# Kernel optimization log

Measured on AMD Instinct MI355X. Metric: run time of the kernel, lower is better.

The kernel has to match this reference:

```python
import jax, jax.numpy as jnp
import numpy as np

B, R, D = 16, 2048, 512
H2, NREL = 2 * D, 2048  # relation_mlp hidden = 2*d_model, output = n_relations
MIN_PROB = 0.1          # early-stop probability threshold from the torch code


def setup_inputs() -> dict:
    key = jax.random.key(0)
    ks = jax.random.split(key, 8)
    sc = lambda k, shp: jax.random.normal(k, shp, jnp.float32) * 0.02
    return {
        "rel_encoding": jax.random.normal(ks[0], (B, R, D), jnp.float32),
        "na_emb": jax.random.normal(ks[1], (D,), jnp.float32),
        "v_w": sc(ks[2], (D, D)), "v_b": jnp.zeros((D,), jnp.float32),
        "o_w": sc(ks[3], (D, D)), "o_b": jnp.zeros((D,), jnp.float32),
        "ln_g": jnp.ones((D,), jnp.float32), "ln_b": jnp.zeros((D,), jnp.float32),
        "w1": sc(ks[4], (H2, D)), "b1": jnp.zeros((H2,), jnp.float32),
        "w2": sc(ks[5], (NREL, H2)), "b2": jnp.zeros((NREL,), jnp.float32),
    }


def _ln(x, g, b, eps=1e-5):
    m = jnp.mean(x, axis=-1, keepdims=True)
    v = jnp.var(x, axis=-1, keepdims=True)
    return (x - m) * jax.lax.rsqrt(v + eps) * g + b


def reference(rel_encoding, na_emb, v_w, v_b, o_w, o_b, ln_g, ln_b, w1, b1, w2, b2):
    # Cross-attention with a single key/value token: softmax over a length-1 axis
    # is identically 1, so attn_out = out_proj(v_proj(kv)) for every query position.
    x = rel_encoding                                         # [B,R,D]
    attn = (x @ v_w.T + v_b) @ o_w.T + o_b                   # [B,R,D]

    def step_logits(state):                                  # state broadcasts to [B,R,D]
        h = _ln(attn + state, ln_g, ln_b)                    # residual + layernorm
        return jax.nn.relu(h @ w1.T + b1) @ w2.T + b2        # [B,R,NREL]

    # step 0: query is the na_embedding
    p0 = jax.nn.softmax(step_logits(na_emb), axis=-1)
    m0 = jnp.max(p0, axis=-1)
    i0 = jnp.argmax(p0, axis=-1)
    cont0 = (i0 != 0) & (m0 >= MIN_PROB)                     # else break before step 0 emits

    # step 1: last appended state is the relation encoding itself
    p1 = jax.nn.softmax(step_logits(x), axis=-1)
    m1 = jnp.max(p1, axis=-1)
    i1 = jnp.argmax(p1, axis=-1)
    cont1 = cont0 & (i1 != 0) & (m1 >= MIN_PROB)

    # rule_score = prod of accepted step probs; 0.0 if no step accepted
    scores = jnp.where(cont0, jnp.where(cont1, m0 * m1, m0), 0.0)  # [B,R]
    lengths = cont0.astype(jnp.int32) + cont1.astype(jnp.int32)    # ragged rule lengths
    return scores, i0, i1, lengths
```

## Files before the change

kernel.cpp:

```cpp
#include <hip/hip_runtime.h>
#include <math.h>

#define MTOT 32768
#define DD   512
#define HHD  1024
#define NRELN 2048
#define SCA  64.f
#define SCB  1024.f
#define INVS (1.f / 65536.f)

typedef _Float16 h8  __attribute__((ext_vector_type(8)));
typedef float    f16v __attribute__((ext_vector_type(16)));

__device__ __forceinline__ void fsplit(float x, _Float16& h, _Float16& l) {
  _Float16 t = (_Float16)x;
  h = t;
  l = (_Float16)(x - (float)t);
}

__device__ __forceinline__ void omerge(float& M, float& S, int& I, float m2, float s2, int i2) {
  if (m2 > M || (m2 == M && i2 < I)) { S = S * __expf(M - m2) + s2; M = m2; I = i2; }
  else                               { S += s2 * __expf(m2 - M); }
}

__device__ __forceinline__ void gld16(const _Float16* g, _Float16* l) {
  __builtin_amdgcn_global_load_lds(
      (const __attribute__((address_space(1))) void*)g,
      (__attribute__((address_space(3))) void*)l, 16, 0, 0);
}


__global__ void prep_wvo_split(const float* __restrict__ vw, const float* __restrict__ ow,
                               _Float16* __restrict__ wh, _Float16* __restrict__ wl) {
  int idx = blockIdx.x * 256 + threadIdx.x;
  int k = idx & 511;
  int n = idx >> 9;
  float s = 0.f;
  for (int j = 0; j < DD; ++j) s += ow[n * DD + j] * vw[j * DD + k];
  fsplit(s * SCB, wh[n * DD + k], wl[n * DD + k]);
}

__global__ void prep_cvec(const float* __restrict__ ow, const float* __restrict__ vb,
                          const float* __restrict__ ob, float* __restrict__ c) {
  int i = blockIdx.x * 256 + threadIdx.x;
  if (i < DD) {
    float s = ob[i];
    for (int k = 0; k < DD; ++k) s += ow[i * DD + k] * vb[k];
    c[i] = s;
  }
}

__global__ void prep_w1p_split(const float* __restrict__ w1, const float* __restrict__ g,
                               _Float16* __restrict__ wh, _Float16* __restrict__ wl) {
  int idx = blockIdx.x * 256 + threadIdx.x;
  int k = idx & 511;
  int n = idx >> 9;
  fsplit(w1[n * DD + k] * g[k] * SCB, wh[n * DD + k], wl[n * DD + k]);
}

__global__ void prep_b1p(const float* __restrict__ w1, const float* __restrict__ lnb,
                         const float* __restrict__ b1, float* __restrict__ b1p) {
  int n = blockIdx.x * 256 + threadIdx.x;
  if (n < HHD) {
    float s = b1[n];
    for (int k = 0; k < DD; ++k) s += w1[n * DD + k] * lnb[k];
    b1p[n] = s;
  }
}

__global__ void prep_w2_split(const float* __restrict__ w2,
                              _Float16* __restrict__ wh, _Float16* __restrict__ wl) {
  int idx = blockIdx.x * 256 + threadIdx.x;
  int k = idx & 1023;
  int n = idx >> 10;
  fsplit(w2[n * HHD + k] * SCB, wh[n * HHD + k], wl[n * HHD + k]);
}

__global__ void split_x(const float* __restrict__ src, _Float16* __restrict__ h,
                        _Float16* __restrict__ l) {
  int idx = (blockIdx.x * 256 + threadIdx.x) * 8;
  float4 a = *(const float4*)(src + idx);
  float4 b = *(const float4*)(src + idx + 4);
  float vv[8] = {a.x, a.y, a.z, a.w, b.x, b.y, b.z, b.w};
  _Float16 hh[8], ll[8];
#pragma unroll
  for (int i = 0; i < 8; ++i) fsplit(vv[i] * SCA, hh[i], ll[i]);
  *(h8*)(h + idx) = *(h8*)hh;
  *(h8*)(l + idx) = *(h8*)ll;
}

template <int MODE, int KDIM, int NTOT>
__global__ __launch_bounds__(256) void gemm_split(
    const _Float16* __restrict__ Ah, const _Float16* __restrict__ Al,
    const _Float16* __restrict__ Bh, const _Float16* __restrict__ Bl,
    const float* __restrict__ bias,
    float* __restrict__ outF,
    _Float16* __restrict__ outHh, _Float16* __restrict__ outHl,
    float* __restrict__ pM, float* __restrict__ pS, float* __restrict__ pI,
    int row0) {
  __shared__ __align__(16) _Float16 sA[2][128][32];
  __shared__ __align__(16) _Float16 sB[2][128][32];
  const int t = threadIdx.x;
  const int lane = t & 63;
  const int wv = t >> 6;
  const int wr = wv & 1, wc = wv >> 1;
  const int l31 = lane & 31, half = lane >> 5;
  const int m0 = blockIdx.x << 7;
  const int n0 = blockIdx.y << 7;

  const _Float16* gsp = (wv == 0) ? Ah : (wv == 1) ? Al : (wv == 2) ? Bh : Bl;
  const int gb = (wv < 2) ? m0 : n0;
  _Float16* lbase = (wv == 0) ? &sA[0][0][0] : (wv == 1) ? &sA[1][0][0]
                  : (wv == 2) ? &sB[0][0][0] : &sB[1][0][0];
  const int srow = lane >> 2;
  const int schunk = (lane & 3) ^ ((lane >> 3) & 3);
  const _Float16* gptr0 = gsp + (size_t)(gb + srow) * KDIM + schunk * 8;

  f16v acc[2][2] = {};
  const int swz = (lane >> 1) & 3;

  for (int k0 = 0; k0 < KDIM; k0 += 32) {
    __syncthreads();
#pragma unroll
    for (int it = 0; it < 8; ++it)
      gld16(gptr0 + k0 + (size_t)(it * 16) * KDIM, lbase + it * 512);
    __syncthreads();
#pragma unroll
    for (int ks = 0; ks < 2; ++ks) {
      const int pos = (((ks << 1) + half) ^ swz) << 3;
      h8 af_h[2], af_l[2], bf_h[2], bf_l[2];
#pragma unroll
      for (int i = 0; i < 2; ++i) {
        const int mr = wr * 64 + i * 32 + l31;
        af_h[i] = *(const h8*)&sA[0][mr][pos];
        af_l[i] = *(const h8*)&sA[1][mr][pos];
      }
#pragma unroll
      for (int j = 0; j < 2; ++j) {
        const int nr = wc * 64 + j * 32 + l31;
        bf_h[j] = *(const h8*)&sB[0][nr][pos];
        bf_l[j] = *(const h8*)&sB[1][nr][pos];
      }
#pragma unroll
      for (int j = 0; j < 2; ++j)
#pragma unroll
        for (int i = 0; i < 2; ++i) {
          acc[i][j] = __builtin_amdgcn_mfma_f32_32x32x16_f16(af_h[i], bf_h[j], acc[i][j], 0, 0, 0);
          acc[i][j] = __builtin_amdgcn_mfma_f32_32x32x16_f16(af_h[i], bf_l[j], acc[i][j], 0, 0, 0);
          acc[i][j] = __builtin_amdgcn_mfma_f32_32x32x16_f16(af_l[i], bf_h[j], acc[i][j], 0, 0, 0);
        }
    }
  }

  float bb[2];
  int gc[2];
#pragma unroll
  for (int j = 0; j < 2; ++j) {
    gc[j] = n0 + wc * 64 + j * 32 + l31;
    bb[j] = bias[gc[j]];
  }
  if constexpr (MODE == 0) {
#pragma unroll
    for (int i = 0; i < 2; ++i)
#pragma unroll
      for (int r = 0; r < 16; ++r) {
        const int row = m0 + wr * 64 + i * 32 + (r & 3) + 8 * (r >> 2) + 4 * half;
#pragma unroll
        for (int j = 0; j < 2; ++j)
          outF[(size_t)row * NTOT + gc[j]] = acc[i][j][r] * INVS + bb[j];
      }
  } else if constexpr (MODE == 1) {
#pragma unroll
    for (int i = 0; i < 2; ++i)
#pragma unroll
      for (int r = 0; r < 16; ++r) {
        const int row = m0 + wr * 64 + i * 32 + (r & 3) + 8 * (r >> 2) + 4 * half;
#pragma unroll
        for (int j = 0; j < 2; ++j) {
          float v = fmaxf(acc[i][j][r] * INVS + bb[j], 0.f) * SCA;
          _Float16 hh, ll;
          fsplit(v, hh, ll);
          outHh[(size_t)row * NTOT + gc[j]] = hh;
          outHl[(size_t)row * NTOT + gc[j]] = ll;
        }
      }
  } else {
    const int slot = blockIdx.y * 2 + wc;
#pragma unroll
    for (int i = 0; i < 2; ++i)
#pragma unroll
      for (int r = 0; r < 16; ++r) {
        float v0 = acc[i][0][r] * INVS + bb[0];
        float v1 = acc[i][1][r] * INVS + bb[1];
        float M;
        int I;
        if (v0 >= v1) { M = v0; I = gc[0]; }
        else          { M = v1; I = gc[1]; }
#pragma unroll
        for (int sh = 1; sh <= 16; sh <<= 1) {
          float M2 = __shfl_xor(M, sh);
          int   I2 = __shfl_xor(I, sh);
          if (M2 > M || (M2 == M && I2 < I)) { M = M2; I = I2; }
        }
        float S = __expf(v0 - M) + __expf(v1 - M);
#pragma unroll
        for (int sh = 1; sh <= 16; sh <<= 1) S += __shfl_xor(S, sh);
        if (l31 == 0) {
          const int grow = row0 + m0 + wr * 64 + i * 32 + (r & 3) + 8 * (r >> 2) + 4 * half;
          pM[(size_t)slot * MTOT + grow] = M;
          pS[(size_t)slot * MTOT + grow] = S;
          pI[(size_t)slot * MTOT + grow] = (float)I;
        }
      }
  }
}

__global__ __launch_bounds__(256) void ln_dual(
    const float* __restrict__ A, const float* __restrict__ X,
    const float* __restrict__ na,
    _Float16* __restrict__ y0h, _Float16* __restrict__ y0l,
    _Float16* __restrict__ y1h, _Float16* __restrict__ y1l, int row0) {
  int t = threadIdx.x;
  int lane = t & 63;
  int w = t >> 6;
  int r = blockIdx.x * 4 + w;
  const float* ap = A + (size_t)r * DD + lane * 8;
  const float* xp = X + (size_t)(row0 + r) * DD + lane * 8;
  const float* np = na + lane * 8;
  float v0[8], v1[8];
  float s0 = 0.f, q0 = 0.f, s1 = 0.f, q1 = 0.f;
#pragma unroll
  for (int i = 0; i < 8; ++i) {
    float a = ap[i];
    v0[i] = a + np[i];
    v1[i] = a + xp[i];
    s0 += v0[i]; q0 += v0[i] * v0[i];
    s1 += v1[i]; q1 += v1[i] * v1[i];
  }
#pragma unroll
  for (int m = 1; m <= 32; m <<= 1) {
    s0 += __shfl_xor(s0, m); q0 += __shfl_xor(q0, m);
    s1 += __shfl_xor(s1, m); q1 += __shfl_xor(q1, m);
  }
  float mu0 = s0 * (1.f / DD), mu1 = s1 * (1.f / DD);
  float rs0 = 1.f / sqrtf(q0 * (1.f / DD) - mu0 * mu0 + 1e-5f);
  float rs1 = 1.f / sqrtf(q1 * (1.f / DD) - mu1 * mu1 + 1e-5f);
  _Float16 h0[8], l0[8], h1[8], l1[8];
#pragma unroll
  for (int i = 0; i < 8; ++i) {
    fsplit((v0[i] - mu0) * rs0 * SCA, h0[i], l0[i]);
    fsplit((v1[i] - mu1) * rs1 * SCA, h1[i], l1[i]);
  }
  *(h8*)(y0h + (size_t)r * DD + lane * 8) = *(h8*)h0;
  *(h8*)(y0l + (size_t)r * DD + lane * 8) = *(h8*)l0;
  *(h8*)(y1h + (size_t)r * DD + lane * 8) = *(h8*)h1;
  *(h8*)(y1l + (size_t)r * DD + lane * 8) = *(h8*)l1;
}

__global__ void finalize_k(const float* __restrict__ pM0, const float* __restrict__ pS0,
                           const float* __restrict__ pI0, const float* __restrict__ pM1,
                           const float* __restrict__ pS1, const float* __restrict__ pI1,
                           float* __restrict__ out) {
  int r = blockIdx.x * 256 + threadIdx.x;
  float M = pM0[r], S = pS0[r];
  int I = (int)pI0[r];
  for (int s = 1; s < 32; ++s) {
    size_t o = (size_t)s * MTOT + r;
    omerge(M, S, I, pM0[o], pS0[o], (int)pI0[o]);
  }
  float m0v = 1.f / S;
  int i0v = I;
  M = pM1[r]; S = pS1[r]; I = (int)pI1[r];
  for (int s = 1; s < 32; ++s) {
    size_t o = (size_t)s * MTOT + r;
    omerge(M, S, I, pM1[o], pS1[o], (int)pI1[o]);
  }
  float m1v = 1.f / S;
  int i1v = I;
  bool c0 = (i0v != 0) && (m0v >= 0.1f);
  bool c1 = c0 && (i1v != 0) && (m1v >= 0.1f);
  out[r] = c0 ? (c1 ? m0v * m1v : m0v) : 0.f;
  out[MTOT + r] = (float)i0v;
  out[2 * MTOT + r] = (float)i1v;
  out[3 * MTOT + r] = (float)((c0 ? 1 : 0) + (c1 ? 1 : 0));
}

extern "C" void kernel_launch(void* const* d_in, const int* in_sizes, int n_in,
                              void* d_out, int out_size, void* d_ws, size_t ws_size,
                              hipStream_t stream) {
  const float* X   = (const float*)d_in[0];
  const float* na  = (const float*)d_in[1];
  const float* vw  = (const float*)d_in[2];
  const float* vb  = (const float*)d_in[3];
  const float* ow  = (const float*)d_in[4];
  const float* ob  = (const float*)d_in[5];
  const float* lng = (const float*)d_in[6];
  const float* lnb = (const float*)d_in[7];
  const float* w1  = (const float*)d_in[8];
  const float* b1  = (const float*)d_in[9];
  const float* w2  = (const float*)d_in[10];
  const float* b2  = (const float*)d_in[11];
  float* out = (float*)d_out;

  char* p = (char*)d_ws;
  auto alloc = [&](size_t bytes) -> void* {
    void* r = (void*)p;
    p += (bytes + 255) & ~(size_t)255;
    return r;
  };
  _Float16* wvo_h = (_Float16*)alloc(512 * 512 * 2);
  _Float16* wvo_l = (_Float16*)alloc(512 * 512 * 2);
  float*    cvec  = (float*)alloc(512 * 4);
  _Float16* w1p_h = (_Float16*)alloc(1024 * 512 * 2);
  _Float16* w1p_l = (_Float16*)alloc(1024 * 512 * 2);
  float*    b1p   = (float*)alloc(1024 * 4);
  _Float16* w2_h  = (_Float16*)alloc(2048 * 1024 * 2);
  _Float16* w2_l  = (_Float16*)alloc(2048 * 1024 * 2);
  float* pM0 = (float*)alloc((size_t)32 * MTOT * 4);
  float* pS0 = (float*)alloc((size_t)32 * MTOT * 4);
  float* pI0 = (float*)alloc((size_t)32 * MTOT * 4);
  float* pM1 = (float*)alloc((size_t)32 * MTOT * 4);
  float* pS1 = (float*)alloc((size_t)32 * MTOT * 4);
  float* pI1 = (float*)alloc((size_t)32 * MTOT * 4);
  size_t fixed = (size_t)(p - (char*)d_ws);
  size_t remain = ws_size > fixed + 8192 ? ws_size - fixed - 8192 : 0;
  int chunk = (int)(remain / 10240);
  chunk &= ~127;
  if (chunk < 128) chunk = 128;
  if (chunk > MTOT) chunk = MTOT;
  _Float16* xs_h = (_Float16*)alloc((size_t)chunk * 512 * 2);
  _Float16* xs_l = (_Float16*)alloc((size_t)chunk * 512 * 2);
  float*    Abuf = (float*)alloc((size_t)chunk * 512 * 4);
  _Float16* y0_h = (_Float16*)alloc((size_t)chunk * 512 * 2);
  _Float16* y0_l = (_Float16*)alloc((size_t)chunk * 512 * 2);
  _Float16* H_h  = (_Float16*)alloc((size_t)chunk * 1024 * 2);
  _Float16* H_l  = (_Float16*)alloc((size_t)chunk * 1024 * 2);
  _Float16* y1_h = xs_h;
  _Float16* y1_l = xs_l;

  prep_wvo_split<<<1024, 256, 0, stream>>>(vw, ow, wvo_h, wvo_l);
  prep_cvec<<<2, 256, 0, stream>>>(ow, vb, ob, cvec);
  prep_w1p_split<<<2048, 256, 0, stream>>>(w1, lng, w1p_h, w1p_l);
  prep_b1p<<<4, 256, 0, stream>>>(w1, lnb, b1, b1p);
  prep_w2_split<<<8192, 256, 0, stream>>>(w2, w2_h, w2_l);

  for (int row0 = 0; row0 < MTOT; row0 += chunk) {
    int rows = (MTOT - row0 < chunk) ? (MTOT - row0) : chunk;
    split_x<<<rows / 4, 256, 0, stream>>>(X + (size_t)row0 * 512, xs_h, xs_l);
    gemm_split<0, 512, 512><<<dim3(rows / 128, 4), 256, 0, stream>>>(
        xs_h, xs_l, wvo_h, wvo_l, cvec, Abuf, nullptr, nullptr,
        nullptr, nullptr, nullptr, 0);
    ln_dual<<<rows / 4, 256, 0, stream>>>(Abuf, X, na, y0_h, y0_l, y1_h, y1_l, row0);
    for (int s = 0; s < 2; ++s) {
      gemm_split<1, 512, 1024><<<dim3(rows / 128, 8), 256, 0, stream>>>(
          s == 0 ? y0_h : y1_h, s == 0 ? y0_l : y1_l, w1p_h, w1p_l, b1p,
          nullptr, H_h, H_l, nullptr, nullptr, nullptr, 0);
      gemm_split<2, 1024, 2048><<<dim3(rows / 128, 16), 256, 0, stream>>>(
          H_h, H_l, w2_h, w2_l, b2, nullptr, nullptr, nullptr,
          s == 0 ? pM0 : pM1, s == 0 ? pS0 : pS1, s == 0 ? pI0 : pI1, row0);
    }
  }
  finalize_k<<<MTOT / 256, 256, 0, stream>>>(pM0, pS0, pI0, pM1, pS1, pI1, out);
}
```

Measured before the change: 1.680 ms.

## Compute final GEMM in single fp16, recompute near-tie rows in split precision

The largest GEMM (hidden to relation logits) now runs as one fp16 MFMA pass instead of three split-precision passes. It tracks the top-two logits and the softmax sum per row. Rows whose top-two margin is below a threshold are flagged with an atomic counter, gathered into a compact buffer, and recomputed with the full split-precision GEMM to settle the argmax. Max-probability values still come from the approximate pass, and rescue is capped at a fixed number of rows per chunk, so accuracy depends on logit gaps and the cap. The LDS swizzle also changes, and the final reduction moves into per-chunk flag kernels.

New measurement: 1.635 ms. -2.7%, faster.

```diff
diff --git a/kernel.cpp b/kernel.cpp
--- a/kernel.cpp
+++ b/kernel.cpp
@@ -8,6 +8,8 @@
 #define SCA  64.f
 #define SCB  1024.f
 #define INVS (1.f / 65536.f)
+#define CAPR 4096
+#define MARGIN 2.0e-3f
 
 typedef _Float16 h8  __attribute__((ext_vector_type(8)));
 typedef float    f16v __attribute__((ext_vector_type(16)));
@@ -16,11 +18,6 @@
   _Float16 t = (_Float16)x;
   h = t;
   l = (_Float16)(x - (float)t);
-}
-
-__device__ __forceinline__ void omerge(float& M, float& S, int& I, float m2, float s2, int i2) {
-  if (m2 > M || (m2 == M && i2 < I)) { S = S * __expf(M - m2) + s2; M = m2; I = i2; }
-  else                               { S += s2 * __expf(m2 - M); }
 }
 
 __device__ __forceinline__ void gld16(const _Float16* g, _Float16* l) {
@@ -89,6 +86,8 @@
   *(h8*)(l + idx) = *(h8*)ll;
 }
 
+__global__ void zero_cnt(int* c) { c[blockIdx.x * 256 + threadIdx.x] = 0; }
+
 template <int MODE, int KDIM, int NTOT>
 __global__ __launch_bounds__(256) void gemm_split(
     const _Float16* __restrict__ Ah, const _Float16* __restrict__ Al,
@@ -96,8 +95,8 @@
     const float* __restrict__ bias,
     float* __restrict__ outF,
     _Float16* __restrict__ outHh, _Float16* __restrict__ outHl,
-    float* __restrict__ pM, float* __restrict__ pS, float* __restrict__ pI,
-    int row0) {
+    float* __restrict__ pM, float* __restrict__ pI,
+    const int* __restrict__ cntp, int pstr) {
   __shared__ __align__(16) _Float16 sA[2][128][32];
   __shared__ __align__(16) _Float16 sB[2][128][32];
   const int t = threadIdx.x;
@@ -105,127 +104,299 @@
   const int wv = t >> 6;
   const int wr = wv & 1, wc = wv >> 1;
   const int l31 = lane & 31, half = lane >> 5;
-  const int m0 = blockIdx.x << 7;
   const int n0 = blockIdx.y << 7;
 
   const _Float16* gsp = (wv == 0) ? Ah : (wv == 1) ? Al : (wv == 2) ? Bh : Bl;
-  const int gb = (wv < 2) ? m0 : n0;
   _Float16* lbase = (wv == 0) ? &sA[0][0][0] : (wv == 1) ? &sA[1][0][0]
                   : (wv == 2) ? &sB[0][0][0] : &sB[1][0][0];
   const int srow = lane >> 2;
-  const int schunk = (lane & 3) ^ ((lane >> 3) & 3);
-  const _Float16* gptr0 = gsp + (size_t)(gb + srow) * KDIM + schunk * 8;
-
-  f16v acc[2][2] = {};
-  const int swz = (lane >> 1) & 3;
-
-  for (int k0 = 0; k0 < KDIM; k0 += 32) {
+  const int scp = lane & 3;
+  const int swzE = ((srow >> 1) & 3) ^ ((srow >> 3) & 1);
+  const int swzO = swzE ^ 2;
+  const int swz = ((l31 >> 1) ^ (l31 >> 3)) & 3;
+
+  int nmb;
+  if constexpr (MODE == 2) {
+    int a = *cntp;
+    if (a > CAPR) a = CAPR;
+    nmb = (a + 127) >> 7;
+  } else {
+    nmb = gridDim.x;
+  }
+
+  for (int mb = blockIdx.x; mb < nmb; mb += gridDim.x) {
+    const int m0 = mb << 7;
+    const int gb = (wv < 2) ? m0 : n0;
+    const _Float16* gA0 = gsp + (size_t)(gb + srow) * KDIM + ((scp ^ swzE) << 3);
+    const _Float16* gA1 = gsp + (size_t)(gb + srow) * KDIM + ((scp ^ swzO) << 3);
+
+    f16v acc[2][2] = {};
+    for (int k0 = 0; k0 < KDIM; k0 += 32) {
+      __syncthreads();
+#pragma unroll
+      for (int it = 0; it < 8; ++it)
+        gld16(((it & 1) ? gA1 : gA0) + (size_t)(it * 16) * KDIM + k0, lbase + it * 512);
+      __syncthreads();
+#pragma unroll
+      for (int ks = 0; ks < 2; ++ks) {
+        const int pos = (((ks << 1) + half) ^ swz) << 3;
+        h8 af_h[2], af_l[2], bf_h[2], bf_l[2];
+#pragma unroll
+        for (int i = 0; i < 2; ++i) {
+          const int mr = wr * 64 + i * 32 + l31;
+          af_h[i] = *(const h8*)&sA[0][mr][pos];
+          af_l[i] = *(const h8*)&sA[1][mr][pos];
+        }
+#pragma unroll
+        for (int j = 0; j < 2; ++j) {
+          const int nr = wc * 64 + j * 32 + l31;
+          bf_h[j] = *(const h8*)&sB[0][nr][pos];
+          bf_l[j] = *(const h8*)&sB[1][nr][pos];
+        }
+#pragma unroll
+        for (int j = 0; j < 2; ++j)
+#pragma unroll
+          for (int i = 0; i < 2; ++i) {
+            acc[i][j] = __builtin_amdgcn_mfma_f32_32x32x16_f16(af_h[i], bf_h[j], acc[i][j], 0, 0, 0);
+            acc[i][j] = __builtin_amdgcn_mfma_f32_32x32x16_f16(af_h[i], bf_l[j], acc[i][j], 0, 0, 0);
+            acc[i][j] = __builtin_amdgcn_mfma_f32_32x32x16_f16(af_l[i], bf_h[j], acc[i][j], 0, 0, 0);
+          }
+      }
+    }
+
+    float bb[2];
+    int gc[2];
+#pragma unroll
+    for (int j = 0; j < 2; ++j) {
+      gc[j] = n0 + wc * 64 + j * 32 + l31;
+      bb[j] = bias[gc[j]];
+    }
+    if constexpr (MODE == 0) {
+#pragma unroll
+      for (int i = 0; i < 2; ++i)
+#pragma unroll
+        for (int r = 0; r < 16; ++r) {
+          const int row = m0 + wr * 64 + i * 32 + (r & 3) + 8 * (r >> 2) + 4 * half;
+#pragma unroll
+          for (int j = 0; j < 2; ++j)
+            outF[(size_t)row * NTOT + gc[j]] = acc[i][j][r] * INVS + bb[j];
+        }
+    } else if constexpr (MODE == 1) {
+#pragma unroll
+      for (int i = 0; i < 2; ++i)
+#pragma unroll
+        for (int r = 0; r < 16; ++r) {
+          const int row = m0 + wr * 64 + i * 32 + (r & 3) + 8 * (r >> 2) + 4 * half;
+#pragma unroll
+          for (int j = 0; j < 2; ++j) {
+            float v = fmaxf(acc[i][j][r] * INVS + bb[j], 0.f) * SCA;
+            _Float16 hh, ll;
+            fsplit(v, hh, ll);
+            outHh[(size_t)row * NTOT + gc[j]] = hh;
+            outHl[(size_t)row * NTOT + gc[j]] = ll;
+          }
+        }
+    } else {
+      const int slot = blockIdx.y * 2 + wc;
+#pragma unroll
+      for (int i = 0; i < 2; ++i)
+#pragma unroll
+        for (int r = 0; r < 16; ++r) {
+          float v0 = acc[i][0][r] * INVS + bb[0];
+          float v1 = acc[i][1][r] * INVS + bb[1];
+          float M;
+          int I;
+          if (v0 >= v1) { M = v0; I = gc[0]; }
+          else          { M = v1; I = gc[1]; }
+#pragma unroll
+          for (int sh = 1; sh <= 16; sh <<= 1) {
+            float M2 = __shfl_xor(M, sh);
+            int   I2 = __shfl_xor(I, sh);
+            if (M2 > M || (M2 == M && I2 < I)) { M = M2; I = I2; }
+          }
+          if (l31 == 0) {
+            const int grow = m0 + wr * 64 + i * 32 + (r & 3) + 8 * (r >> 2) + 4 * half;
+            pM[(size_t)slot * pstr + grow] = M;
+            pI[(size_t)slot * pstr + grow] = (float)I;
+          }
+        }
+    }
+  }
+}
+
+__global__ __launch_bounds__(256) void gemm_approx(
+    const _Float16* __restrict__ Ah, const _Float16* __restrict__ Bh,
+    const float* __restrict__ bias,
+    float* __restrict__ pM, float* __restrict__ pM2,
+    float* __restrict__ pS, int* __restrict__ pI, int astr) {
+  __shared__ __align__(16) _Float16 sAB[12288];
+  const int t = threadIdx.x;
+  const int lane = t & 63;
+  const int wv = t >> 6;
+  const int wr = wv & 1, wc = wv >> 1;
+  const int l31 = lane & 31, half = lane >> 5;
+  const int m0 = blockIdx.x << 7;
+  const int n0 = blockIdx.y << 8;
+
+  const _Float16* gsrc[6];
+  _Float16* ldst[6];
+#pragma unroll
+  for (int it = 0; it < 6; ++it) {
+    int p = (it * 4 + wv) * 64 + lane;
+    const _Float16* s;
+    if (p < 512) {
+      int row = p >> 2, cp = p & 3;
+      int sw = ((row >> 1) ^ (row >> 3)) & 3;
+      s = Ah + (size_t)(m0 + row) * HHD + ((cp ^ sw) << 3);
+    } else {
+      int pq = p - 512;
+      int row = pq >> 2, cp = pq & 3;
+      int sw = ((row >> 1) ^ (row >> 3)) & 3;
+      s = Bh + (size_t)(n0 + row) * HHD + ((cp ^ sw) << 3);
+    }
+    gsrc[it] = s;
+    ldst[it] = sAB + (size_t)(it * 4 + wv) * 512;
+  }
+  const int swz = ((l31 >> 1) ^ (l31 >> 3)) & 3;
+
+  f16v acc[2][4] = {};
+  for (int k0 = 0; k0 < HHD; k0 += 32) {
     __syncthreads();
 #pragma unroll
-    for (int it = 0; it < 8; ++it)
-      gld16(gptr0 + k0 + (size_t)(it * 16) * KDIM, lbase + it * 512);
+    for (int it = 0; it < 6; ++it) gld16(gsrc[it] + k0, ldst[it]);
     __syncthreads();
 #pragma unroll
     for (int ks = 0; ks < 2; ++ks) {
       const int pos = (((ks << 1) + half) ^ swz) << 3;
-      h8 af_h[2], af_l[2], bf_h[2], bf_l[2];
-#pragma unroll
-      for (int i = 0; i < 2; ++i) {
-        const int mr = wr * 64 + i * 32 + l31;
-        af_h[i] = *(const h8*)&sA[0][mr][pos];
-        af_l[i] = *(const h8*)&sA[1][mr][pos];
+      h8 af[2], bf[4];
+#pragma unroll
+      for (int i = 0; i < 2; ++i)
+        af[i] = *(const h8*)&sAB[(size_t)(wr * 64 + i * 32 + l31) * 32 + pos];
+#pragma unroll
+      for (int j = 0; j < 4; ++j)
+        bf[j] = *(const h8*)&sAB[4096 + (size_t)(wc * 128 + j * 32 + l31) * 32 + pos];
+#pragma unroll
+      for (int j = 0; j < 4; ++j)
+#pragma unroll
+        for (int i = 0; i < 2; ++i)
+          acc[i][j] = __builtin_amdgcn_mfma_f32_32x32x16_f16(af[i], bf[j], acc[i][j], 0, 0, 0);
+    }
+  }
+
+  const int slot = blockIdx.y * 2 + wc;
+  float bb[4];
+  int gc[4];
+#pragma unroll
+  for (int j = 0; j < 4; ++j) {
+    gc[j] = n0 + wc * 128 + j * 32 + l31;
+    bb[j] = bias[gc[j]];
+  }
+#pragma unroll
+  for (int i = 0; i < 2; ++i)
+#pragma unroll
+    for (int r = 0; r < 16; ++r) {
+      float M = acc[i][0][r] * INVS + bb[0], M2 = -INFINITY, S = 1.f;
+      int I = gc[0];
+#pragma unroll
+      for (int j = 1; j < 4; ++j) {
+        float v = acc[i][j][r] * INVS + bb[j];
+        if (v > M || (v == M && gc[j] < I)) {
+          S = S * __expf(M - v) + 1.f; M2 = M; M = v; I = gc[j];
+        } else {
+          S += __expf(v - M); M2 = fmaxf(M2, v);
+        }
       }
 #pragma unroll
-      for (int j = 0; j < 2; ++j) {
-        const int nr = wc * 64 + j * 32 + l31;
-        bf_h[j] = *(const h8*)&sB[0][nr][pos];
-        bf_l[j] = *(const h8*)&sB[1][nr][pos];
+      for (int sh = 1; sh <= 16; sh <<= 1) {
+        float Mo = __shfl_xor(M, sh);
+        float M2o = __shfl_xor(M2, sh);
+        float So = __shfl_xor(S, sh);
+        int   Io = __shfl_xor(I, sh);
+        if (Mo > M || (Mo == M && Io < I)) {
+          S = S * __expf(M - Mo) + So; M2 = fmaxf(M, M2o); M = Mo; I = Io;
+        } else {
+          S += So * __expf(Mo - M); M2 = fmaxf(M2, Mo);
+        }
       }
-#pragma unroll
-      for (int j = 0; j < 2; ++j)
-#pragma unroll
-        for (int i = 0; i < 2; ++i) {
-          acc[i][j] = __builtin_amdgcn_mfma_f32_32x32x16_f16(af_h[i], bf_h[j], acc[i][j], 0, 0, 0);
-          acc[i][j] = __builtin_amdgcn_mfma_f32_32x32x16_f16(af_h[i], bf_l[j], acc[i][j], 0, 0, 0);
-          acc[i][j] = __builtin_amdgcn_mfma_f32_32x32x16_f16(af_l[i], bf_h[j], acc[i][j], 0, 0, 0);
-        }
-    }
-  }
-
-  float bb[2];
-  int gc[2];
-#pragma unroll
-  for (int j = 0; j < 2; ++j) {
-    gc[j] = n0 + wc * 64 + j * 32 + l31;
-    bb[j] = bias[gc[j]];
-  }
-  if constexpr (MODE == 0) {
-#pragma unroll
-    for (int i = 0; i < 2; ++i)
-#pragma unroll
-      for (int r = 0; r < 16; ++r) {
-        const int row = m0 + wr * 64 + i * 32 + (r & 3) + 8 * (r >> 2) + 4 * half;
-#pragma unroll
-        for (int j = 0; j < 2; ++j)
-          outF[(size_t)row * NTOT + gc[j]] = acc[i][j][r] * INVS + bb[j];
+      if (l31 == 0) {
+        const int grow = m0 + wr * 64 + i * 32 + (r & 3) + 8 * (r >> 2) + 4 * half;
+        pM[(size_t)slot * astr + grow] = M;
+        pM2[(size_t)slot * astr + grow] = M2;
+        pS[(size_t)slot * astr + grow] = S;
+        pI[(size_t)slot * astr + grow] = I;
       }
-  } else if constexpr (MODE == 1) {
-#pragma unroll
-    for (int i = 0; i < 2; ++i)
-#pragma unroll
-      for (int r = 0; r < 16; ++r) {
-        const int row = m0 + wr * 64 + i * 32 + (r & 3) + 8 * (r >> 2) + 4 * half;
-#pragma unroll
-        for (int j = 0; j < 2; ++j) {
-          float v = fmaxf(acc[i][j][r] * INVS + bb[j], 0.f) * SCA;
-          _Float16 hh, ll;
-          fsplit(v, hh, ll);
-          outHh[(size_t)row * NTOT + gc[j]] = hh;
-          outHl[(size_t)row * NTOT + gc[j]] = ll;
-        }
-      }
-  } else {
-    const int slot = blockIdx.y * 2 + wc;
-#pragma unroll
-    for (int i = 0; i < 2; ++i)
-#pragma unroll
-      for (int r = 0; r < 16; ++r) {
-        float v0 = acc[i][0][r] * INVS + bb[0];
-        float v1 = acc[i][1][r] * INVS + bb[1];
-        float M;
-        int I;
-        if (v0 >= v1) { M = v0; I = gc[0]; }
-        else          { M = v1; I = gc[1]; }
-#pragma unroll
-        for (int sh = 1; sh <= 16; sh <<= 1) {
-          float M2 = __shfl_xor(M, sh);
-          int   I2 = __shfl_xor(I, sh);
-          if (M2 > M || (M2 == M && I2 < I)) { M = M2; I = I2; }
-        }
-        float S = __expf(v0 - M) + __expf(v1 - M);
-#pragma unroll
-        for (int sh = 1; sh <= 16; sh <<= 1) S += __shfl_xor(S, sh);
-        if (l31 == 0) {
-          const int grow = row0 + m0 + wr * 64 + i * 32 + (r & 3) + 8 * (r >> 2) + 4 * half;
-          pM[(size_t)slot * MTOT + grow] = M;
-          pS[(size_t)slot * MTOT + grow] = S;
-          pI[(size_t)slot * MTOT + grow] = (float)I;
-        }
-      }
-  }
+    }
+}
+
+__global__ void flag_k(const float* __restrict__ pM, const float* __restrict__ pM2,
+                       const float* __restrict__ pS, const int* __restrict__ pI,
+                       int astr, int rows,
+                       float* __restrict__ map, int* __restrict__ iap, int row0,
+                       int* __restrict__ list, int* __restrict__ cnt) {
+  int r = blockIdx.x * 256 + threadIdx.x;
+  if (r >= rows) return;
+  float M = pM[r], M2 = pM2[r], S = pS[r];
+  int I = pI[r];
+  for (int s = 1; s < 16; ++s) {
+    size_t o = (size_t)s * astr + r;
+    float m = pM[o], m2 = pM2[o], ss = pS[o];
+    int ii = pI[o];
+    if (m > M || (m == M && ii < I)) {
+      M2 = fmaxf(M, m2); S = S * __expf(M - m) + ss; M = m; I = ii;
+    } else {
+      M2 = fmaxf(M2, m); S += ss * __expf(m - M);
+    }
+  }
+  map[row0 + r] = 1.f / S;
+  iap[row0 + r] = I;
+  if (M - M2 < MARGIN) {
+    int c = atomicAdd(cnt, 1);
+    if (c < CAPR) list[c] = r;
+  }
+}
+
+__global__ void gather_k(const _Float16* __restrict__ Hh, const _Float16* __restrict__ Hl,
+                         const int* __restrict__ list, const int* __restrict__ cnt,
+                         _Float16* __restrict__ Gh, _Float16* __restrict__ Gl) {
+  int b = blockIdx.x;
+  int active = *cnt;
+  if (active > CAPR) active = CAPR;
+  if (b >= active) return;
+  int r = list[b];
+  int t = threadIdx.x;
+  *(h8*)(Gh + (size_t)b * HHD + t * 8) = *(const h8*)(Hh + (size_t)r * HHD + t * 8);
+  *(h8*)(Gl + (size_t)b * HHD + t * 8) = *(const h8*)(Hl + (size_t)r * HHD + t * 8);
+}
+
+__global__ void rescue_merge(const float* __restrict__ pMr, const float* __restrict__ pIr,
+                             const int* __restrict__ list, const int* __restrict__ cnt,
+                             int* __restrict__ iap, int row0) {
+  int c = blockIdx.x * 256 + threadIdx.x;
+  int a = *cnt;
+  if (a > CAPR) a = CAPR;
+  if (c >= a) return;
+  float M = pMr[c];
+  int I = (int)pIr[c];
+  for (int s = 1; s < 32; ++s) {
+    size_t o = (size_t)s * CAPR + c;
+    float m = pMr[o];
+    int i2 = (int)pIr[o];
+    if (m > M || (m == M && i2 < I)) { M = m; I = i2; }
+  }
+  iap[row0 + list[c]] = I;
 }
 
 __global__ __launch_bounds__(256) void ln_dual(
     const float* __restrict__ A, const float* __restrict__ X,
     const float* __restrict__ na,
     _Float16* __restrict__ y0h, _Float16* __restrict__ y0l,
-    _Float16* __restrict__ y1h, _Float16* __restrict__ y1l, int row0) {
+    _Float16* __restrict__ y1h, _Float16* __restrict__ y1l) {
   int t = threadIdx.x;
   int lane = t & 63;
   int w = t >> 6;
   int r = blockIdx.x * 4 + w;
   const float* ap = A + (size_t)r * DD + lane * 8;
-  const float* xp = X + (size_t)(row0 + r) * DD + lane * 8;
+  const float* xp = X + (size_t)r * DD + lane * 8;
   const float* np = na + lane * 8;
   float v0[8], v1[8];
   float s0 = 0.f, q0 = 0.f, s1 = 0.f, q1 = 0.f;
@@ -257,26 +428,12 @@
   *(h8*)(y1l + (size_t)r * DD + lane * 8) = *(h8*)l1;
 }
 
-__global__ void finalize_k(const float* __restrict__ pM0, const float* __restrict__ pS0,
-                           const float* __restrict__ pI0, const float* __restrict__ pM1,
-                           const float* __restrict__ pS1, const float* __restrict__ pI1,
+__global__ void finalize_k(const float* __restrict__ map0, const int* __restrict__ iap0,
+                           const float* __restrict__ map1, const int* __restrict__ iap1,
                            float* __restrict__ out) {
   int r = blockIdx.x * 256 + threadIdx.x;
-  float M = pM0[r], S = pS0[r];
-  int I = (int)pI0[r];
-  for (int s = 1; s < 32; ++s) {
-    size_t o = (size_t)s * MTOT + r;
-    omerge(M, S, I, pM0[o], pS0[o], (int)pI0[o]);
-  }
-  float m0v = 1.f / S;
-  int i0v = I;
-  M = pM1[r]; S = pS1[r]; I = (int)pI1[r];
-  for (int s = 1; s < 32; ++s) {
-    size_t o = (size_t)s * MTOT + r;
-    omerge(M, S, I, pM1[o], pS1[o], (int)pI1[o]);
-  }
-  float m1v = 1.f / S;
-  int i1v = I;
+  float m0v = map0[r], m1v = map1[r];
+  int i0v = iap0[r], i1v = iap1[r];
   bool c0 = (i0v != 0) && (m0v >= 0.1f);
   bool c1 = c0 && (i1v != 0) && (m1v >= 0.1f);
   out[r] = c0 ? (c1 ? m0v * m1v : m0v) : 0.f;
@@ -316,18 +473,25 @@
   float*    b1p   = (float*)alloc(1024 * 4);
   _Float16* w2_h  = (_Float16*)alloc(2048 * 1024 * 2);
   _Float16* w2_l  = (_Float16*)alloc(2048 * 1024 * 2);
-  float* pM0 = (float*)alloc((size_t)32 * MTOT * 4);
-  float* pS0 = (float*)alloc((size_t)32 * MTOT * 4);
-  float* pI0 = (float*)alloc((size_t)32 * MTOT * 4);
-  float* pM1 = (float*)alloc((size_t)32 * MTOT * 4);
-  float* pS1 = (float*)alloc((size_t)32 * MTOT * 4);
-  float* pI1 = (float*)alloc((size_t)32 * MTOT * 4);
+  float* map0 = (float*)alloc((size_t)MTOT * 4);
+  float* map1 = (float*)alloc((size_t)MTOT * 4);
+  int* iap0 = (int*)alloc((size_t)MTOT * 4);
+  int* iap1 = (int*)alloc((size_t)MTOT * 4);
+  int* list = (int*)alloc(CAPR * 4);
+  int* cnt  = (int*)alloc(512 * 4);
+  float* pMr = (float*)alloc((size_t)32 * CAPR * 4);
+  float* pIr = (float*)alloc((size_t)32 * CAPR * 4);
+  _Float16* Gh = (_Float16*)alloc((size_t)CAPR * HHD * 2);
+  _Float16* Gl = (_Float16*)alloc((size_t)CAPR * HHD * 2);
+
   size_t fixed = (size_t)(p - (char*)d_ws);
-  size_t remain = ws_size > fixed + 8192 ? ws_size - fixed - 8192 : 0;
-  int chunk = (int)(remain / 10240);
+  size_t reserve = 2u << 20;
+  size_t remain = ws_size > fixed + reserve ? ws_size - fixed - reserve : 0;
+  int chunk = (int)(remain / 10496);
   chunk &= ~127;
   if (chunk < 128) chunk = 128;
   if (chunk > MTOT) chunk = MTOT;
+
   _Float16* xs_h = (_Float16*)alloc((size_t)chunk * 512 * 2);
   _Float16* xs_l = (_Float16*)alloc((size_t)chunk * 512 * 2);
   float*    Abuf = (float*)alloc((size_t)chunk * 512 * 4);
@@ -335,30 +499,46 @@
   _Float16* y0_l = (_Float16*)alloc((size_t)chunk * 512 * 2);
   _Float16* H_h  = (_Float16*)alloc((size_t)chunk * 1024 * 2);
   _Float16* H_l  = (_Float16*)alloc((size_t)chunk * 1024 * 2);
+  float* pMa  = (float*)alloc((size_t)16 * chunk * 4);
+  float* pM2a = (float*)alloc((size_t)16 * chunk * 4);
+  float* pSa  = (float*)alloc((size_t)16 * chunk * 4);
+  int*   pIa  = (int*)alloc((size_t)16 * chunk * 4);
   _Float16* y1_h = xs_h;
   _Float16* y1_l = xs_l;
 
+  zero_cnt<<<2, 256, 0, stream>>>(cnt);
   prep_wvo_split<<<1024, 256, 0, stream>>>(vw, ow, wvo_h, wvo_l);
   prep_cvec<<<2, 256, 0, stream>>>(ow, vb, ob, cvec);
   prep_w1p_split<<<2048, 256, 0, stream>>>(w1, lng, w1p_h, w1p_l);
   prep_b1p<<<4, 256, 0, stream>>>(w1, lnb, b1, b1p);
   prep_w2_split<<<8192, 256, 0, stream>>>(w2, w2_h, w2_l);
 
-  for (int row0 = 0; row0 < MTOT; row0 += chunk) {
+  int citer = 0;
+  for (int row0 = 0; row0 < MTOT; row0 += chunk, ++citer) {
     int rows = (MTOT - row0 < chunk) ? (MTOT - row0) : chunk;
-    split_x<<<rows / 4, 256, 0, stream>>>(X + (size_t)row0 * 512, xs_h, xs_l);
+    split_x<<<rows * 512 / 2048, 256, 0, stream>>>(X + (size_t)row0 * 512, xs_h, xs_l);
     gemm_split<0, 512, 512><<<dim3(rows / 128, 4), 256, 0, stream>>>(
         xs_h, xs_l, wvo_h, wvo_l, cvec, Abuf, nullptr, nullptr,
         nullptr, nullptr, nullptr, 0);
-    ln_dual<<<rows / 4, 256, 0, stream>>>(Abuf, X, na, y0_h, y0_l, y1_h, y1_l, row0);
+    ln_dual<<<rows / 4, 256, 0, stream>>>(Abuf, X + (size_t)row0 * 512, na,
+                                          y0_h, y0_l, y1_h, y1_l);
     for (int s = 0; s < 2; ++s) {
+      int* cp = cnt + citer * 2 + s;
       gemm_split<1, 512, 1024><<<dim3(rows / 128, 8), 256, 0, stream>>>(
           s == 0 ? y0_h : y1_h, s == 0 ? y0_l : y1_l, w1p_h, w1p_l, b1p,
           nullptr, H_h, H_l, nullptr, nullptr, nullptr, 0);
-      gemm_split<2, 1024, 2048><<<dim3(rows / 128, 16), 256, 0, stream>>>(
-          H_h, H_l, w2_h, w2_l, b2, nullptr, nullptr, nullptr,
-          s == 0 ? pM0 : pM1, s == 0 ? pS0 : pS1, s == 0 ? pI0 : pI1, row0);
-    }
-  }
-  finalize_k<<<MTOT / 256, 256, 0, stream>>>(pM0, pS0, pI0, pM1, pS1, pI1, out);
-}
+      gemm_approx<<<dim3(rows / 128, 8), 256, 0, stream>>>(
+          H_h, w2_h, b2, pMa, pM2a, pSa, pIa, chunk);
+      flag_k<<<(rows + 255) / 256, 256, 0, stream>>>(
+          pMa, pM2a, pSa, pIa, chunk, rows,
+          s == 0 ? map0 : map1, s == 0 ? iap0 : iap1, row0, list, cp);
+      gather_k<<<CAPR, 128, 0, stream>>>(H_h, H_l, list, cp, Gh, Gl);
+      gemm_split<2, 1024, 2048><<<dim3(8, 16), 256, 0, stream>>>(
+          Gh, Gl, w2_h, w2_l, b2, nullptr, nullptr, nullptr,
+          pMr, pIr, cp, CAPR);
+      rescue_merge<<<CAPR / 256, 256, 0, stream>>>(
+          pMr, pIr, list, cp, s == 0 ? iap0 : iap1, row0);
+    }
+  }
+  finalize_k<<<MTOT / 256, 256, 0, stream>>>(map0, iap0, map1, iap1, out);
+}
```
